# Kernel tuning notes

Hardware: AMD Instinct MI355X
Metric: run time of the kernel (lower is better)

The kernel has to match this reference:

```python
import jax, jax.numpy as jnp
import numpy as np

WS = 7          # window_size
N = WS * WS     # 49 tokens per window
DIM = 384
H = 12
HD = DIM // H   # 32
NW = 64         # windows per image (mask leading dim)


def _rel_pos_index():
    coords = np.stack(np.meshgrid(np.arange(WS), np.arange(WS), indexing='ij'))  # (2, WS, WS)
    cf = coords.reshape(2, -1)                      # (2, N)
    rel = cf[:, :, None] - cf[:, None, :]           # (2, N, N)
    rel = rel.transpose(1, 2, 0)                    # (N, N, 2)
    idx = (rel[..., 0] + WS - 1) * (2 * WS - 1) + (rel[..., 1] + WS - 1)
    return jnp.asarray(idx, dtype=jnp.int32)        # (N, N)

REL_IDX = _rel_pos_index()


def setup_inputs() -> dict:
    key = jax.random.key(0)
    ks = jax.random.split(key, 10)
    B_ = 2048
    x = jax.random.normal(ks[0], (B_, N, DIM), dtype=jnp.float32)
    mask = jnp.zeros((NW, N, N), dtype=jnp.float32)
    s = 0.02
    Wq = jax.random.normal(ks[1], (DIM, DIM), jnp.float32) * s
    Wk = jax.random.normal(ks[2], (DIM, DIM), jnp.float32) * s
    Wv = jax.random.normal(ks[3], (DIM, DIM), jnp.float32) * s
    Wp = jax.random.normal(ks[4], (DIM, DIM), jnp.float32) * s
    bq = jnp.zeros((DIM,), jnp.float32)
    bk = jnp.zeros((DIM,), jnp.float32)
    bv = jnp.zeros((DIM,), jnp.float32)
    bp = jnp.zeros((DIM,), jnp.float32)
    table = jax.random.normal(ks[5], ((2 * WS - 1) ** 2, H), jnp.float32) * s
    return {"x": x, "mask": mask, "Wq": Wq, "bq": bq, "Wk": Wk, "bk": bk,
            "Wv": Wv, "bv": bv, "Wp": Wp, "bp": bp, "table": table}


def reference(x, mask, Wq, bq, Wk, bk, Wv, bv, Wp, bp, table):
    b_, n, c = x.shape
    scale = HD ** (-0.5)
    # projections: PyTorch Linear is x @ W.T + b
    q = (x @ Wq.T + bq).reshape(b_, n, H, HD).transpose(0, 2, 1, 3)  # (B, H, N, D)
    k = (x @ Wk.T + bk).reshape(b_, n, H, HD).transpose(0, 2, 1, 3)
    v = (x @ Wv.T + bv).reshape(b_, n, H, HD).transpose(0, 2, 1, 3)
    attn = jnp.einsum('bhnd,bhmd->bhnm', q * scale, k)               # (B, H, N, N)
    rel_bias = table[REL_IDX]                                        # (N, N, H)
    attn = attn + rel_bias.transpose(2, 0, 1)[None]                  # broadcast over B
    # mask add: (B//nW, nW, H, N, N) + mask[None, :, None]
    nw = mask.shape[0]
    attn = attn.reshape(b_ // nw, nw, H, n, n) + mask[None, :, None]
    attn = attn.reshape(b_, H, n, n)
    attn = jax.nn.softmax(attn, axis=-1)
    out = jnp.einsum('bhnm,bhmd->bhnd', attn, v)                     # (B, H, N, D)
    out = out.transpose(0, 2, 1, 3).reshape(b_, n, c)
    return out @ Wp.T + bp
```

## Files before the change

kernel.cpp:

```cpp
#include <hip/hip_runtime.h>
#include <stdint.h>

using bf16x8 = __attribute__((ext_vector_type(8))) short;
using f32x4  = __attribute__((ext_vector_type(4))) float;

__device__ __forceinline__ short f2bf(float f) {
  uint32_t u = __float_as_uint(f);
  u += 0x7fff + ((u >> 16) & 1u);
  return (short)(u >> 16);
}

#define MFMA16(a, b, c) __builtin_amdgcn_mfma_f32_16x16x32_bf16((a), (b), (c), 0, 0, 0)

__device__ __forceinline__ void gl_lds16(const short* g, short* l) {
  __builtin_amdgcn_global_load_lds(
      (const __attribute__((address_space(1))) void*)g,
      (__attribute__((address_space(3))) void*)l, 16, 0, 0);
}

__global__ void prep_w(const float* __restrict__ Wq, const float* __restrict__ bq,
                       const float* __restrict__ Wk, const float* __restrict__ bk,
                       const float* __restrict__ Wv, const float* __restrict__ bv,
                       const float* __restrict__ Wp, const float* __restrict__ bp,
                       short* __restrict__ Wqkv, short* __restrict__ Wpb,
                       float* __restrict__ bqkv, float* __restrict__ bpb) {
  int i = blockIdx.x * 256 + threadIdx.x;
  const float scale = 0.17677669529663687f;
  if (i < 1152 * 384) {
    int r = i / 384, k = i - r * 384;
    float v;
    if (r < 384)      v = Wq[r * 384 + k] * scale;
    else if (r < 768) v = Wk[(r - 384) * 384 + k];
    else              v = Wv[(r - 768) * 384 + k];
    Wqkv[i] = f2bf(v);
  }
  if (i < 384 * 384) Wpb[i] = f2bf(Wp[i]);
  if (i < 1152) bqkv[i] = (i < 384) ? bq[i] * scale : ((i < 768) ? bk[i - 384] : bv[i - 768]);
  if (i < 384) bpb[i] = bp[i];
}

__global__ void prep_bm(const float* __restrict__ table, const float* __restrict__ mask,
                        float* __restrict__ bmL, int nwmask) {
  int wm = blockIdx.x / 12, h = blockIdx.x - wm * 12;
  const float* mrow = mask + (size_t)wm * 2401;
  float* dst = bmL + (size_t)blockIdx.x * 4096;
  for (int e = threadIdx.x; e < 4096; e += 256) {
    int mn = e >> 8, c = (e >> 4) & 15, i = e & 15;
    int row = (mn >> 2) * 16 + i, col = (mn & 3) * 16 + c;
    float v = -3.0e38f;
    if (row < 49 && col < 49) {
      int id = row / 7, ir = row - id * 7;
      int jd = col / 7, jr = col - jd * 7;
      int idx = (id - jd + 6) * 13 + (ir - jr + 6);
      v = table[idx * 12 + h] + mrow[row * 49 + col];
    }
    dst[e] = v;
  }
}

__global__ void prep_x(const float* __restrict__ x, short* __restrict__ xb, int n8) {
  int u = blockIdx.x * 256 + threadIdx.x;
  if (u < n8) {
    int e = u * 8;
    float4 f0 = *(const float4*)(x + e);
    float4 f1 = *(const float4*)(x + e + 4);
    bf16x8 cv;
    cv[0] = f2bf(f0.x); cv[1] = f2bf(f0.y); cv[2] = f2bf(f0.z); cv[3] = f2bf(f0.w);
    cv[4] = f2bf(f1.x); cv[5] = f2bf(f1.y); cv[6] = f2bf(f1.z); cv[7] = f2bf(f1.w);
    *(bf16x8*)(xb + e) = cv;
  }
}

__global__ __launch_bounds__(256) void qkv_gemm(
    const short* __restrict__ xb, const short* __restrict__ Wqkv,
    const float* __restrict__ bqkv,
    short* __restrict__ qws, short* __restrict__ kws, short* __restrict__ vws,
    int ntok) {
  __shared__ __align__(16) short smem[2 * 320 * 64];
  const int tid = threadIdx.x;
  const int lane = tid & 63, wv = tid >> 6;
  const int c = lane & 15, g = lane >> 4;

  const int mt = gridDim.y;
  int id = blockIdx.y * 6 + blockIdx.x;
  int mt8 = mt & ~7;
  int xq, yq;
  if (id < 6 * mt8) {
    int q = id / 48, r = id - q * 48;
    yq = q * 8 + (r & 7);
    xq = r >> 3;
  } else {
    int rem = id - 6 * mt8;
    xq = rem % 6;
    yq = mt8 + rem / 6;
  }
  const int n0 = xq * 192;
  const int row0 = yq * 128;

  f32x4 acc[8][3];
  const f32x4 zero = {0.f, 0.f, 0.f, 0.f};
#pragma unroll
  for (int m = 0; m < 8; m++)
#pragma unroll
    for (int nn = 0; nn < 3; nn++) acc[m][nn] = zero;

  const int rsub = lane >> 3;
  const int chnk = ((lane & 7) ^ rsub) * 8;
  const short* aS[4];
  const short* bS[6];
#pragma unroll
  for (int i = 0; i < 4; i++) {
    int r = (wv * 4 + i) * 8 + rsub;
    int grow = row0 + r;
    if (grow >= ntok) grow = ntok - 1;
    aS[i] = xb + (size_t)grow * 384 + chnk;
  }
#pragma unroll
  for (int j = 0; j < 6; j++) {
    int r = (wv * 6 + j) * 8 + rsub;
    bS[j] = Wqkv + (size_t)(n0 + r) * 384 + chnk;
  }

  auto stage = [&](int buf, int ks) {
    short* Asl = smem + buf * (320 * 64);
    short* Bsl = Asl + 128 * 64;
#pragma unroll
    for (int i = 0; i < 4; i++)
      gl_lds16(aS[i] + ks * 64, Asl + (wv * 4 + i) * 512);
#pragma unroll
    for (int j = 0; j < 6; j++)
      gl_lds16(bS[j] + ks * 64, Bsl + (wv * 6 + j) * 512);
  };

  stage(0, 0);
  asm volatile("s_waitcnt vmcnt(0)" ::: "memory");
  __builtin_amdgcn_s_barrier();
#pragma unroll
  for (int ks = 0; ks < 6; ks++) {
    const int cur = ks & 1;
    if (ks < 5) {
      stage(cur ^ 1, ks + 1);
      asm volatile("s_waitcnt vmcnt(10)" ::: "memory");
    } else {
      asm volatile("s_waitcnt vmcnt(0)" ::: "memory");
    }
    __builtin_amdgcn_sched_barrier(0);
    __builtin_amdgcn_s_barrier();
    const short* Asl = smem + cur * (320 * 64);
    const short* Bsl = Asl + 128 * 64;
#pragma unroll
    for (int kk = 0; kk < 2; kk++) {
      bf16x8 af[8];
#pragma unroll
      for (int m = 0; m < 8; m++) {
        int row = m * 16 + c;
        af[m] = *(const bf16x8*)&Asl[row * 64 + (((kk * 4 + g) ^ (row & 7)) * 8)];
      }
#pragma unroll
      for (int nn = 0; nn < 3; nn++) {
        int row = wv * 48 + nn * 16 + c;
        bf16x8 bfr = *(const bf16x8*)&Bsl[row * 64 + (((kk * 4 + g) ^ (row & 7)) * 8)];
#pragma unroll
        for (int m = 0; m < 8; m++) acc[m][nn] = MFMA16(af[m], bfr, acc[m][nn]);
      }
    }
    __builtin_amdgcn_sched_barrier(0);
    __builtin_amdgcn_s_barrier();
  }

  const int s = n0 / 384;
  short* base = (s == 0) ? qws : ((s == 1) ? kws : vws);
  const int hbase = (n0 - s * 384) >> 5;
#pragma unroll
  for (int half = 0; half < 2; half++) {
    __syncthreads();
#pragma unroll
    for (int nn = 0; nn < 3; nn++) {
      int colRel = wv * 48 + nn * 16 + c;
      float bias = bqkv[n0 + colRel];
#pragma unroll
      for (int mm = 0; mm < 4; mm++) {
        int m = half * 4 + mm;
#pragma unroll
        for (int r = 0; r < 4; r++)
          smem[(mm * 16 + g * 4 + r) * 200 + colRel] = f2bf(acc[m][nn][r] + bias);
      }
    }
    __syncthreads();
    for (int u = tid; u < 384; u += 256) {
      int row = u & 63, j = u >> 6;
      int tr = row0 + half * 64 + row;
      if (tr < ntok) {
        int bw = tr / 49;
        int n = tr - bw * 49;
        short* dst = base + ((size_t)(bw * 12 + hbase + j) * 49 + n) * 32;
        const uint4* src = (const uint4*)&smem[row * 200 + j * 32];
        uint4* d4 = (uint4*)dst;
        d4[0] = src[0]; d4[1] = src[1]; d4[2] = src[2]; d4[3] = src[3];
      }
    }
  }
}

__global__ __launch_bounds__(256) void attn_kernel(
    const short* __restrict__ qws, const short* __restrict__ kws,
    const short* __restrict__ vws, short* __restrict__ ows,
    const float* __restrict__ bm, int b0, int nwmask) {
  __shared__ short Pall[4 * 64 * 72];
  const int tid = threadIdx.x;
  const int lane = tid & 63, wvi = tid >> 6;
  const int c = lane & 15, g = lane >> 4;
  const int task = blockIdx.x * 4 + wvi;
  const int b = task / 12, h = task - b * 12;
  const int wm = (b0 + b) % nwmask;
  const short* qb = qws + (size_t)(b * 12 + h) * 1568;
  const short* kb = kws + (size_t)(b * 12 + h) * 1568;
  const short* vb = vws + (size_t)(b * 12 + h) * 1568;

  bf16x8 qf[4], kf[4];
#pragma unroll
  for (int m = 0; m < 4; m++) { int i = m * 16 + c; if (i > 48) i = 48; qf[m] = *(const bf16x8*)(qb + i * 32 + g * 8); }
#pragma unroll
  for (int n = 0; n < 4; n++) { int j = n * 16 + c; if (j > 48) j = 48; kf[n] = *(const bf16x8*)(kb + j * 32 + g * 8); }

  bf16x8 vfr[2][2];
#pragma unroll
  for (int kk = 0; kk < 2; kk++)
#pragma unroll
    for (int dt = 0; dt < 2; dt++) {
      bf16x8 vf;
#pragma unroll
      for (int rr = 0; rr < 8; rr++) {
        int j = kk * 32 + g * 8 + rr; if (j > 48) j = 48;
        vf[rr] = vb[j * 32 + dt * 16 + c];
      }
      vfr[kk][dt] = vf;
    }

  const f32x4 zero = {0.f, 0.f, 0.f, 0.f};
  f32x4 S[4][4];
  __builtin_amdgcn_s_setprio(1);
#pragma unroll
  for (int m = 0; m < 4; m++)
#pragma unroll
    for (int n = 0; n < 4; n++) S[m][n] = MFMA16(qf[m], kf[n], zero);
  __builtin_amdgcn_s_setprio(0);

  const float* bmh = bm + (size_t)(wm * 12 + h) * 4096;
#pragma unroll
  for (int m = 0; m < 4; m++)
#pragma unroll
    for (int n = 0; n < 4; n++) {
      f32x4 b4 = *(const f32x4*)(bmh + ((m * 4 + n) * 16 + c) * 16 + g * 4);
      S[m][n][0] += b4[0]; S[m][n][1] += b4[1];
      S[m][n][2] += b4[2]; S[m][n][3] += b4[3];
    }

  float rv[4][4];
  short* P = Pall + wvi * 4608;
#pragma unroll
  for (int m = 0; m < 4; m++)
#pragma unroll
    for (int r = 0; r < 4; r++) {
      float mx = fmaxf(fmaxf(S[m][0][r], S[m][1][r]), fmaxf(S[m][2][r], S[m][3][r]));
      mx = fmaxf(mx, __shfl_xor(mx, 1));
      mx = fmaxf(mx, __shfl_xor(mx, 2));
      mx = fmaxf(mx, __shfl_xor(mx, 4));
      mx = fmaxf(mx, __shfl_xor(mx, 8));
      float e0 = __expf(S[m][0][r] - mx);
      float e1 = __expf(S[m][1][r] - mx);
      float e2 = __expf(S[m][2][r] - mx);
      float e3 = __expf(S[m][3][r] - mx);
      float sm = (e0 + e1) + (e2 + e3);
      sm += __shfl_xor(sm, 1);
      sm += __shfl_xor(sm, 2);
      sm += __shfl_xor(sm, 4);
      sm += __shfl_xor(sm, 8);
      rv[m][r] = 1.0f / sm;
      int row = m * 16 + g * 4 + r;
      P[row * 72 + c]      = f2bf(e0);
      P[row * 72 + 16 + c] = f2bf(e1);
      P[row * 72 + 32 + c] = f2bf(e2);
      P[row * 72 + 48 + c] = f2bf(e3);
    }

  f32x4 O[4][2];
#pragma unroll
  for (int m = 0; m < 4; m++) { O[m][0] = zero; O[m][1] = zero; }
#pragma unroll
  for (int kk = 0; kk < 2; kk++) {
    bf16x8 pf[4];
#pragma unroll
    for (int m = 0; m < 4; m++) pf[m] = *(const bf16x8*)&P[(m * 16 + c) * 72 + kk * 32 + g * 8];
    __builtin_amdgcn_s_setprio(1);
#pragma unroll
    for (int dt = 0; dt < 2; dt++)
#pragma unroll
      for (int m = 0; m < 4; m++) O[m][dt] = MFMA16(pf[m], vfr[kk][dt], O[m][dt]);
    __builtin_amdgcn_s_setprio(0);
  }
#pragma unroll
  for (int m = 0; m < 4; m++)
#pragma unroll
    for (int r = 0; r < 4; r++) {
      int i = m * 16 + g * 4 + r;
      if (i < 49) {
        size_t o = ((size_t)b * 49 + i) * 384 + h * 32;
        ows[o + c]      = f2bf(O[m][0][r] * rv[m][r]);
        ows[o + 16 + c] = f2bf(O[m][1][r] * rv[m][r]);
      }
    }
}

__global__ __launch_bounds__(256) void proj_gemm(
    const short* __restrict__ ows, const short* __restrict__ Wpb,
    const float* __restrict__ bpb, float* __restrict__ out,
    long tok0, int ntok) {
  __shared__ __align__(16) short smem[2 * 320 * 64];
  const int tid = threadIdx.x;
  const int lane = tid & 63, wv = tid >> 6;
  const int c = lane & 15, g = lane >> 4;

  const int mt = gridDim.y;
  int id = blockIdx.y * 2 + blockIdx.x;
  int mt8 = mt & ~7;
  int xq, yq;
  if (id < 2 * mt8) {
    int q = id / 16, r = id - q * 16;
    yq = q * 8 + (r & 7);
    xq = r >> 3;
  } else {
    int rem = id - 2 * mt8;
    xq = rem % 2;
    yq = mt8 + rem / 2;
  }
  const int n0 = xq * 192;
  const int row0 = yq * 128;

  f32x4 acc[8][3];
  const f32x4 zero = {0.f, 0.f, 0.f, 0.f};
#pragma unroll
  for (int m = 0; m < 8; m++)
#pragma unroll
    for (int nn = 0; nn < 3; nn++) acc[m][nn] = zero;

  const int rsub = lane >> 3;
  const int chnk = ((lane & 7) ^ rsub) * 8;
  const short* aS[4];
  const short* bS[6];
#pragma unroll
  for (int i = 0; i < 4; i++) {
    int r = (wv * 4 + i) * 8 + rsub;
    int grow = row0 + r;
    if (grow >= ntok) grow = ntok - 1;
    aS[i] = ows + (size_t)grow * 384 + chnk;
  }
#pragma unroll
  for (int j = 0; j < 6; j++) {
    int r = (wv * 6 + j) * 8 + rsub;
    bS[j] = Wpb + (size_t)(n0 + r) * 384 + chnk;
  }

  auto stage = [&](int buf, int ks) {
    short* Asl = smem + buf * (320 * 64);
    short* Bsl = Asl + 128 * 64;
#pragma unroll
    for (int i = 0; i < 4; i++)
      gl_lds16(aS[i] + ks * 64, Asl + (wv * 4 + i) * 512);
#pragma unroll
    for (int j = 0; j < 6; j++)
      gl_lds16(bS[j] + ks * 64, Bsl + (wv * 6 + j) * 512);
  };

  stage(0, 0);
  asm volatile("s_waitcnt vmcnt(0)" ::: "memory");
  __builtin_amdgcn_s_barrier();
#pragma unroll
  for (int ks = 0; ks < 6; ks++) {
    const int cur = ks & 1;
    if (ks < 5) {
      stage(cur ^ 1, ks + 1);
      asm volatile("s_waitcnt vmcnt(10)" ::: "memory");
    } else {
      asm volatile("s_waitcnt vmcnt(0)" ::: "memory");
    }
    __builtin_amdgcn_sched_barrier(0);
    __builtin_amdgcn_s_barrier();
    const short* Asl = smem + cur * (320 * 64);
    const short* Bsl = Asl + 128 * 64;
#pragma unroll
    for (int kk = 0; kk < 2; kk++) {
      bf16x8 af[8];
#pragma unroll
      for (int m = 0; m < 8; m++) {
        int row = m * 16 + c;
        af[m] = *(const bf16x8*)&Asl[row * 64 + (((kk * 4 + g) ^ (row & 7)) * 8)];
      }
#pragma unroll
      for (int nn = 0; nn < 3; nn++) {
        int row = wv * 48 + nn * 16 + c;
        bf16x8 bfr = *(const bf16x8*)&Bsl[row * 64 + (((kk * 4 + g) ^ (row & 7)) * 8)];
#pragma unroll
        for (int m = 0; m < 8; m++) acc[m][nn] = MFMA16(af[m], bfr, acc[m][nn]);
      }
    }
    __builtin_amdgcn_sched_barrier(0);
    __builtin_amdgcn_s_barrier();
  }
#pragma unroll
  for (int nn = 0; nn < 3; nn++) {
    int cg = n0 + wv * 48 + nn * 16 + c;
    float bias = bpb[cg];
#pragma unroll
    for (int m = 0; m < 8; m++)
#pragma unroll
      for (int r = 0; r < 4; r++) {
        int tr = row0 + m * 16 + g * 4 + r;
        if (tr < ntok) out[((size_t)(tok0 + tr)) * 384 + cg] = acc[m][nn][r] + bias;
      }
  }
}

extern "C" void kernel_launch(void* const* d_in, const int* in_sizes, int n_in,
                              void* d_out, int out_size, void* d_ws, size_t ws_size,
                              hipStream_t stream) {
  const float* x    = (const float*)d_in[0];
  const float* mask = (const float*)d_in[1];
  const float* Wq = (const float*)d_in[2];
  const float* bq = (const float*)d_in[3];
  const float* Wk = (const float*)d_in[4];
  const float* bk = (const float*)d_in[5];
  const float* Wv = (const float*)d_in[6];
  const float* bv = (const float*)d_in[7];
  const float* Wp = (const float*)d_in[8];
  const float* bp = (const float*)d_in[9];
  const float* table = (const float*)d_in[10];
  float* out = (float*)d_out;

  const int Btot = in_sizes[0] / (49 * 384);
  const int NWm  = in_sizes[1] / (49 * 49);

  char* ws = (char*)d_ws;
  short* Wqkv = (short*)ws;
  short* Wpb  = Wqkv + 1152 * 384;
  float* bqkv = (float*)(Wpb + 384 * 384);
  float* bpb  = bqkv + 1152;
  float* bmp  = bpb + 384;
  size_t fixedB = (size_t)(1152 * 384 + 384 * 384) * 2 + (1152 + 384) * 4
                + (size_t)NWm * 12 * 4096 * 4;
  char* dyn = ws + ((fixedB + 255) & ~(size_t)255);
  size_t used = (size_t)(dyn - ws);
  size_t avail = (ws_size > used + 4096) ? (ws_size - used - 4096) : 0;
  const size_t perw = (size_t)5 * 18816 * 2;
  long nwc = (long)(avail / perw);
  if (nwc > Btot) nwc = Btot;
  if (nwc >= 64) nwc &= ~63L;
  if (nwc < 1) nwc = 1;
  short* xbw = (short*)dyn;
  short* qws = xbw + (size_t)nwc * 18816;
  short* kws = qws + (size_t)nwc * 18816;
  short* vws = kws + (size_t)nwc * 18816;
  short* ows = vws + (size_t)nwc * 18816;

  prep_w<<<dim3(1728), dim3(256), 0, stream>>>(Wq, bq, Wk, bk, Wv, bv, Wp, bp,
                                               Wqkv, Wpb, bqkv, bpb);
  prep_bm<<<dim3(NWm * 12), dim3(256), 0, stream>>>(table, mask, bmp, NWm);

  for (long b0 = 0; b0 < Btot; b0 += nwc) {
    int nw = (int)((Btot - b0 < nwc) ? (Btot - b0) : nwc);
    int ntok = nw * 49;
    long tok0 = b0 * 49;
    int n8 = ntok * 48;
    prep_x<<<dim3((n8 + 255) / 256), dim3(256), 0, stream>>>(x + tok0 * 384, xbw, n8);
    int mt = (ntok + 127) / 128;
    qkv_gemm<<<dim3(6, mt), dim3(256), 0, stream>>>(xbw, Wqkv, bqkv, qws, kws, vws, ntok);
    attn_kernel<<<dim3(3 * nw), dim3(256), 0, stream>>>(qws, kws, vws, ows, bmp,
                                                        (int)b0, NWm);
    proj_gemm<<<dim3(2, mt), dim3(256), 0, stream>>>(ows, Wpb, bpb, out, tok0, ntok);
  }
}
```

Measured before the change: 589.5 us.

## Fuse x bf16 conversion into QKV GEMM, transpose attention scores, stage projection stores

Removes the separate prep_x pass by having qkv_gemm load fp32 x into registers, convert it to bf16 and write it to LDS within the double-buffered loop. The attention kernel now computes S transposed (K·Q), so each softmax row lives in a lane group that reduces across g. This needs only two cross-lane shuffles, and normalization is applied to P before the PV product instead of to the output. The projection epilogue stages fp32 results through LDS to emit coalesced float4 stores. The cost is that each QKV workgroup re-reads and re-converts the fp32 A tile, which increases its global read traffic, but the prep_x read/write round trip goes away.

```diff
diff --git a/kernel.cpp b/kernel.cpp
--- a/kernel.cpp
+++ b/kernel.cpp
@@ -40,13 +40,14 @@
 }
 
 __global__ void prep_bm(const float* __restrict__ table, const float* __restrict__ mask,
-                        float* __restrict__ bmL, int nwmask) {
+                        float* __restrict__ bmT, int nwmask) {
   int wm = blockIdx.x / 12, h = blockIdx.x - wm * 12;
   const float* mrow = mask + (size_t)wm * 2401;
-  float* dst = bmL + (size_t)blockIdx.x * 4096;
+  float* dst = bmT + (size_t)blockIdx.x * 4096;
   for (int e = threadIdx.x; e < 4096; e += 256) {
-    int mn = e >> 8, c = (e >> 4) & 15, i = e & 15;
-    int row = (mn >> 2) * 16 + i, col = (mn & 3) * 16 + c;
+    int mn = e >> 8, cf = (e >> 4) & 15, if_ = e & 15;
+    int row = (mn >> 2) * 16 + cf;
+    int col = (mn & 3) * 16 + if_;
     float v = -3.0e38f;
     if (row < 49 && col < 49) {
       int id = row / 7, ir = row - id * 7;
@@ -58,21 +59,8 @@
   }
 }
 
-__global__ void prep_x(const float* __restrict__ x, short* __restrict__ xb, int n8) {
-  int u = blockIdx.x * 256 + threadIdx.x;
-  if (u < n8) {
-    int e = u * 8;
-    float4 f0 = *(const float4*)(x + e);
-    float4 f1 = *(const float4*)(x + e + 4);
-    bf16x8 cv;
-    cv[0] = f2bf(f0.x); cv[1] = f2bf(f0.y); cv[2] = f2bf(f0.z); cv[3] = f2bf(f0.w);
-    cv[4] = f2bf(f1.x); cv[5] = f2bf(f1.y); cv[6] = f2bf(f1.z); cv[7] = f2bf(f1.w);
-    *(bf16x8*)(xb + e) = cv;
-  }
-}
-
 __global__ __launch_bounds__(256) void qkv_gemm(
-    const short* __restrict__ xb, const short* __restrict__ Wqkv,
+    const float* __restrict__ xf, const short* __restrict__ Wqkv,
     const float* __restrict__ bqkv,
     short* __restrict__ qws, short* __restrict__ kws, short* __restrict__ vws,
     int ntok) {
@@ -105,47 +93,64 @@
     for (int nn = 0; nn < 3; nn++) acc[m][nn] = zero;
 
   const int rsub = lane >> 3;
-  const int chnk = ((lane & 7) ^ rsub) * 8;
-  const short* aS[4];
-  const short* bS[6];
+  const int tchk = lane & 7;
+  const int chnkB = ((lane & 7) ^ rsub) * 8;
+
+  const float* aF[4];
+  int aoff[4];
 #pragma unroll
   for (int i = 0; i < 4; i++) {
     int r = (wv * 4 + i) * 8 + rsub;
     int grow = row0 + r;
     if (grow >= ntok) grow = ntok - 1;
-    aS[i] = xb + (size_t)grow * 384 + chnk;
-  }
+    aF[i] = xf + (size_t)grow * 384 + tchk * 8;
+    aoff[i] = r * 64 + ((tchk ^ rsub) * 8);
+  }
+  const short* bS[6];
 #pragma unroll
   for (int j = 0; j < 6; j++) {
     int r = (wv * 6 + j) * 8 + rsub;
-    bS[j] = Wqkv + (size_t)(n0 + r) * 384 + chnk;
-  }
-
-  auto stage = [&](int buf, int ks) {
+    bS[j] = Wqkv + (size_t)(n0 + r) * 384 + chnkB;
+  }
+
+  float4 a0[4], a1[4];
+  auto loadA = [&](int ks) {
+#pragma unroll
+    for (int i = 0; i < 4; i++) {
+      a0[i] = *(const float4*)(aF[i] + ks * 64);
+      a1[i] = *(const float4*)(aF[i] + ks * 64 + 4);
+    }
+  };
+  auto writeA = [&](int buf) {
     short* Asl = smem + buf * (320 * 64);
-    short* Bsl = Asl + 128 * 64;
-#pragma unroll
-    for (int i = 0; i < 4; i++)
-      gl_lds16(aS[i] + ks * 64, Asl + (wv * 4 + i) * 512);
+#pragma unroll
+    for (int i = 0; i < 4; i++) {
+      bf16x8 cv;
+      cv[0] = f2bf(a0[i].x); cv[1] = f2bf(a0[i].y);
+      cv[2] = f2bf(a0[i].z); cv[3] = f2bf(a0[i].w);
+      cv[4] = f2bf(a1[i].x); cv[5] = f2bf(a1[i].y);
+      cv[6] = f2bf(a1[i].z); cv[7] = f2bf(a1[i].w);
+      *(bf16x8*)&Asl[aoff[i]] = cv;
+    }
+  };
+  auto stageB = [&](int buf, int ks) {
+    short* Bsl = smem + buf * (320 * 64) + 128 * 64;
 #pragma unroll
     for (int j = 0; j < 6; j++)
       gl_lds16(bS[j] + ks * 64, Bsl + (wv * 6 + j) * 512);
   };
 
-  stage(0, 0);
-  asm volatile("s_waitcnt vmcnt(0)" ::: "memory");
-  __builtin_amdgcn_s_barrier();
+  loadA(0);
+  stageB(0, 0);
+  writeA(0);
+  __syncthreads();
 #pragma unroll
   for (int ks = 0; ks < 6; ks++) {
     const int cur = ks & 1;
     if (ks < 5) {
-      stage(cur ^ 1, ks + 1);
-      asm volatile("s_waitcnt vmcnt(10)" ::: "memory");
-    } else {
-      asm volatile("s_waitcnt vmcnt(0)" ::: "memory");
-    }
-    __builtin_amdgcn_sched_barrier(0);
-    __builtin_amdgcn_s_barrier();
+      loadA(ks + 1);
+      stageB(cur ^ 1, ks + 1);
+    }
     const short* Asl = smem + cur * (320 * 64);
     const short* Bsl = Asl + 128 * 64;
 #pragma unroll
@@ -164,8 +169,8 @@
         for (int m = 0; m < 8; m++) acc[m][nn] = MFMA16(af[m], bfr, acc[m][nn]);
       }
     }
-    __builtin_amdgcn_sched_barrier(0);
-    __builtin_amdgcn_s_barrier();
+    if (ks < 5) writeA(cur ^ 1);
+    __syncthreads();
   }
 
   const int s = n0 / 384;
@@ -243,7 +248,7 @@
 #pragma unroll
   for (int m = 0; m < 4; m++)
 #pragma unroll
-    for (int n = 0; n < 4; n++) S[m][n] = MFMA16(qf[m], kf[n], zero);
+    for (int n = 0; n < 4; n++) S[m][n] = MFMA16(kf[n], qf[m], zero);
   __builtin_amdgcn_s_setprio(0);
 
   const float* bmh = bm + (size_t)(wm * 12 + h) * 4096;
@@ -256,33 +261,35 @@
       S[m][n][2] += b4[2]; S[m][n][3] += b4[3];
     }
 
-  float rv[4][4];
   short* P = Pall + wvi * 4608;
 #pragma unroll
-  for (int m = 0; m < 4; m++)
-#pragma unroll
-    for (int r = 0; r < 4; r++) {
-      float mx = fmaxf(fmaxf(S[m][0][r], S[m][1][r]), fmaxf(S[m][2][r], S[m][3][r]));
-      mx = fmaxf(mx, __shfl_xor(mx, 1));
-      mx = fmaxf(mx, __shfl_xor(mx, 2));
-      mx = fmaxf(mx, __shfl_xor(mx, 4));
-      mx = fmaxf(mx, __shfl_xor(mx, 8));
-      float e0 = __expf(S[m][0][r] - mx);
-      float e1 = __expf(S[m][1][r] - mx);
-      float e2 = __expf(S[m][2][r] - mx);
-      float e3 = __expf(S[m][3][r] - mx);
-      float sm = (e0 + e1) + (e2 + e3);
-      sm += __shfl_xor(sm, 1);
-      sm += __shfl_xor(sm, 2);
-      sm += __shfl_xor(sm, 4);
-      sm += __shfl_xor(sm, 8);
-      rv[m][r] = 1.0f / sm;
-      int row = m * 16 + g * 4 + r;
-      P[row * 72 + c]      = f2bf(e0);
-      P[row * 72 + 16 + c] = f2bf(e1);
-      P[row * 72 + 32 + c] = f2bf(e2);
-      P[row * 72 + 48 + c] = f2bf(e3);
-    }
+  for (int m = 0; m < 4; m++) {
+    float mx = fmaxf(
+        fmaxf(fmaxf(fmaxf(S[m][0][0], S[m][0][1]), fmaxf(S[m][0][2], S[m][0][3])),
+              fmaxf(fmaxf(S[m][1][0], S[m][1][1]), fmaxf(S[m][1][2], S[m][1][3]))),
+        fmaxf(fmaxf(fmaxf(S[m][2][0], S[m][2][1]), fmaxf(S[m][2][2], S[m][2][3])),
+              fmaxf(fmaxf(S[m][3][0], S[m][3][1]), fmaxf(S[m][3][2], S[m][3][3]))));
+    mx = fmaxf(mx, __shfl_xor(mx, 16));
+    mx = fmaxf(mx, __shfl_xor(mx, 32));
+    float e[4][4];
+    float sm = 0.f;
+#pragma unroll
+    for (int n = 0; n < 4; n++)
+#pragma unroll
+      for (int r = 0; r < 4; r++) { e[n][r] = __expf(S[m][n][r] - mx); sm += e[n][r]; }
+    sm += __shfl_xor(sm, 16);
+    sm += __shfl_xor(sm, 32);
+    float rv = 1.0f / sm;
+#pragma unroll
+    for (int n = 0; n < 4; n++) {
+      uint32_t w0 = (uint32_t)(uint16_t)f2bf(e[n][0] * rv) |
+                    ((uint32_t)(uint16_t)f2bf(e[n][1] * rv) << 16);
+      uint32_t w1 = (uint32_t)(uint16_t)f2bf(e[n][2] * rv) |
+                    ((uint32_t)(uint16_t)f2bf(e[n][3] * rv) << 16);
+      uint2 w; w.x = w0; w.y = w1;
+      *(uint2*)&P[(m * 16 + c) * 72 + n * 16 + g * 4] = w;
+    }
+  }
 
   f32x4 O[4][2];
 #pragma unroll
@@ -306,8 +313,8 @@
       int i = m * 16 + g * 4 + r;
       if (i < 49) {
         size_t o = ((size_t)b * 49 + i) * 384 + h * 32;
-        ows[o + c]      = f2bf(O[m][0][r] * rv[m][r]);
-        ows[o + 16 + c] = f2bf(O[m][1][r] * rv[m][r]);
+        ows[o + c]      = f2bf(O[m][0][r]);
+        ows[o + 16 + c] = f2bf(O[m][1][r]);
       }
     }
 }
@@ -407,17 +414,33 @@
     __builtin_amdgcn_sched_barrier(0);
     __builtin_amdgcn_s_barrier();
   }
-#pragma unroll
-  for (int nn = 0; nn < 3; nn++) {
-    int cg = n0 + wv * 48 + nn * 16 + c;
-    float bias = bpb[cg];
-#pragma unroll
-    for (int m = 0; m < 8; m++)
-#pragma unroll
-      for (int r = 0; r < 4; r++) {
-        int tr = row0 + m * 16 + g * 4 + r;
-        if (tr < ntok) out[((size_t)(tok0 + tr)) * 384 + cg] = acc[m][nn][r] + bias;
-      }
+
+  float* fs = (float*)smem;
+#pragma unroll
+  for (int half = 0; half < 2; half++) {
+    __syncthreads();
+#pragma unroll
+    for (int nn = 0; nn < 3; nn++) {
+      int colRel = wv * 48 + nn * 16 + c;
+      float bias = bpb[n0 + colRel];
+#pragma unroll
+      for (int mm = 0; mm < 4; mm++) {
+        int m = half * 4 + mm;
+#pragma unroll
+        for (int r = 0; r < 4; r++)
+          fs[(mm * 16 + g * 4 + r) * 196 + colRel] = acc[m][nn][r] + bias;
+      }
+    }
+    __syncthreads();
+#pragma unroll
+    for (int t = 0; t < 12; t++) {
+      int v = tid + t * 256;
+      int row = v / 48, c4 = v - row * 48;
+      int tr = row0 + half * 64 + row;
+      if (tr < ntok)
+        *(float4*)&out[(size_t)(tok0 + tr) * 384 + n0 + c4 * 4] =
+            *(const float4*)&fs[row * 196 + c4 * 4];
+    }
   }
 }
 
@@ -451,13 +474,12 @@
   char* dyn = ws + ((fixedB + 255) & ~(size_t)255);
   size_t used = (size_t)(dyn - ws);
   size_t avail = (ws_size > used + 4096) ? (ws_size - used - 4096) : 0;
-  const size_t perw = (size_t)5 * 18816 * 2;
+  const size_t perw = (size_t)4 * 18816 * 2;
   long nwc = (long)(avail / perw);
   if (nwc > Btot) nwc = Btot;
   if (nwc >= 64) nwc &= ~63L;
   if (nwc < 1) nwc = 1;
-  short* xbw = (short*)dyn;
-  short* qws = xbw + (size_t)nwc * 18816;
+  short* qws = (short*)dyn;
   short* kws = qws + (size_t)nwc * 18816;
   short* vws = kws + (size_t)nwc * 18816;
   short* ows = vws + (size_t)nwc * 18816;
@@ -470,10 +492,9 @@
     int nw = (int)((Btot - b0 < nwc) ? (Btot - b0) : nwc);
     int ntok = nw * 49;
     long tok0 = b0 * 49;
-    int n8 = ntok * 48;
-    prep_x<<<dim3((n8 + 255) / 256), dim3(256), 0, stream>>>(x + tok0 * 384, xbw, n8);
     int mt = (ntok + 127) / 128;
-    qkv_gemm<<<dim3(6, mt), dim3(256), 0, stream>>>(xbw, Wqkv, bqkv, qws, kws, vws, ntok);
+    qkv_gemm<<<dim3(6, mt), dim3(256), 0, stream>>>(x + tok0 * 384, Wqkv, bqkv,
+                                                    qws, kws, vws, ntok);
     attn_kernel<<<dim3(3 * nw), dim3(256), 0, stream>>>(qws, kws, vws, ows, bmp,
                                                         (int)b0, NWm);
     proj_gemm<<<dim3(2, mt), dim3(256), 0, stream>>>(ows, Wpb, bpb, out, tok0, ntok);
```

Result: faster. 570.5 us (-3.2%).
